# Kernel tuning notes

Hardware: AMD Instinct MI355X
Metric: run time of the kernel (lower is better)

## Reference

```python
import jax, jax.numpy as jnp
import numpy as np

# ---- structural constants (mirror e3nn SO3.tensor_productRs bookkeeping) ----
MUL = 2                      # multiplicity of every irrep in Rs_in / Rs_out
LS = [0, 1, 2]               # irrep orders present in Rs_in and Rs_out
L_MAX = 2                    # spherical-harmonics cutoff -> Y_dim = 9
N_BASIS, HIDDEN = 64, 64     # radial model sizes
R_MAX, GAMMA = 3.5, 4.0      # gaussian radial basis params


def _filter_paths():
    """One entry (l_filter) per (mul_out, mul_in, l_in, l_out, l_f) path."""
    paths = []
    for l_in in LS:
        for l_out in LS:
            for lf in range(abs(l_in - l_out), min(l_in + l_out, L_MAX) + 1):
                paths.extend([lf] * (MUL * MUL))  # mul_in * mul_out copies
    return paths  # len == n_path == 60


def _build_mix_matrices():
    """rf_mix[K, n_path]: broadcast each radial path weight over its 2l+1 components.
    ylm_mix[K, 9]: select Y_{l,m} for each filter component. Both 0/1, block sparse."""
    paths = _filter_paths()
    n_path = len(paths)
    K = sum(2 * l + 1 for l in paths)          # 204
    y_off = {0: 0, 1: 1, 2: 4}                 # offset of l-block inside Y (dim 9)
    rf = np.zeros((K, n_path), dtype=np.float32)
    ylm = np.zeros((K, 9), dtype=np.float32)
    k = 0
    for p, l in enumerate(paths):
        for m in range(2 * l + 1):
            rf[k, p] = 1.0
            ylm[k, y_off[l] + m] = 1.0
            k += 1
    return rf, ylm, n_path, K


def _sh_l012(n):
    """Real spherical harmonics l=0..2 on unit vectors n[Z,3] -> Y[9, Z]."""
    x, y, z = n[:, 0], n[:, 1], n[:, 2]
    c0 = 0.28209479177387814   # 1/(2 sqrt(pi))
    c1 = 0.4886025119029199    # sqrt(3/(4 pi))
    c2a = 1.0925484305920792   # sqrt(15/(4 pi))
    c2b = 0.31539156525252005  # sqrt(5/(16 pi))
    c2c = 0.5462742152960396   # sqrt(15/(16 pi))
    one = jnp.ones_like(x)
    return jnp.stack([
        c0 * one,
        c1 * y, c1 * z, c1 * x,
        c2a * x * y, c2a * y * z, c2b * (3.0 * z * z - 1.0), c2a * x * z,
        c2c * (x * x - y * y),
    ], axis=0)


def setup_inputs() -> dict:
    key = jax.random.key(0)
    k_r, k_cg, k_w1, k_w2 = jax.random.split(key, 4)
    Z = 65536
    D = MUL * sum(2 * l + 1 for l in LS)       # 18 (dim_in == dim_out)
    rf_np, ylm_np, n_path, K = _build_mix_matrices()
    r = 2.0 * jax.random.normal(k_r, (Z, 3), dtype=jnp.float32)
    cg = jax.random.normal(k_cg, (K, D, D), dtype=jnp.float32) / np.sqrt(K)
    W1 = jax.random.normal(k_w1, (N_BASIS, HIDDEN), dtype=jnp.float32) / np.sqrt(N_BASIS)
    b1 = jnp.zeros((HIDDEN,), dtype=jnp.float32)
    W2 = jax.random.normal(k_w2, (HIDDEN, n_path), dtype=jnp.float32) / np.sqrt(HIDDEN)
    b2 = jnp.zeros((n_path,), dtype=jnp.float32)
    return {"r": r, "W1": W1, "b1": b1, "W2": W2, "b2": b2,
            "cg": cg, "rf_mix": jnp.asarray(rf_np), "ylm_mix": jnp.asarray(ylm_np)}


def reference(r, W1, b1, W2, b2, cg, rf_mix, ylm_mix):
    radii = jnp.linalg.norm(r, axis=1)                    # [Z]
    n = r / (radii[:, None] + 1e-12)                      # unit directions
    Y = _sh_l012(n)                                       # [9, Z]  (sh returns [m, ...])
    centers = jnp.linspace(0.0, R_MAX, N_BASIS, dtype=jnp.float32)
    B = jnp.exp(-GAMMA * (radii[:, None] - centers) ** 2) # gaussian radial basis [Z, 64]
    R = jax.nn.relu(B @ W1 + b1) @ W2 + b2                # RadialModel -> [Z, n_path]
    Rm = jnp.einsum('kp,zp->zk', rf_mix, R)               # 'ij,zj->zi'
    Ym = jnp.einsum('ky,yz->zk', ylm_mix, Y)              # 'ij,jz->zi'
    # 'kij,zk,zk->zij' : fuse the two per-point vectors, then one GEMM over k
    kernel = jnp.einsum('kij,zk->zij', cg, Rm * Ym)       # [Z, 18, 18]
    return kernel
```

## Files before the change

kernel.cpp:

```cpp
#include <hip/hip_runtime.h>

#define NPATH 60
#define KDIM  204
#define KPAD  224
#define NIJ   324
#define NTIL  21
#define HID   64

#define BHS   88
#define CLS   232

typedef short bf16x8 __attribute__((ext_vector_type(8)));
typedef float f32x4  __attribute__((ext_vector_type(4)));

__device__ __align__(16) unsigned short g_w1s[4096];
__device__ __align__(16) unsigned short g_w2s[4096];
__device__ __align__(16) unsigned short g_cgs[75264];
__device__ unsigned int  g_pyk[112];

__device__ inline unsigned short f2bf(float f) {
    unsigned int u = __builtin_bit_cast(unsigned int, f);
    u += 0x7fffu + ((u >> 16) & 1u);
    return (unsigned short)(u >> 16);
}
__device__ inline float bf2f(unsigned short h) {
    unsigned int u = ((unsigned int)h) << 16;
    return __builtin_bit_cast(float, u);
}

__global__ void prep_kernel(const float* __restrict__ W1, const float* __restrict__ W2,
                            const float* __restrict__ cg, const float* __restrict__ rf,
                            const float* __restrict__ ylm)
{
    int idx = blockIdx.x * 256 + threadIdx.x;
    if (idx < 4096) {
        int e = idx & 7, ln = (idx >> 3) & 63, nt = (idx >> 9) & 3, kc = idx >> 11;
        int k = kc * 32 + (ln >> 4) * 8 + e;
        int n = nt * 16 + (ln & 15);
        g_w1s[idx] = f2bf(W1[k * HID + n]);
    } else if (idx < 8192) {
        int j = idx - 4096;
        int e = j & 7, ln = (j >> 3) & 63, nt = (j >> 9) & 3, kc = j >> 11;
        int k = kc * 32 + (ln >> 4) * 8 + e;
        int n = nt * 16 + (ln & 15);
        g_w2s[j] = f2bf(n < NPATH ? W2[k * NPATH + n] : 0.0f);
    } else if (idx < 8192 + 75264) {
        int j = idx - 8192;
        int e = j & 7, ln = (j >> 3) & 63;
        int nt = (j >> 9) % NTIL;
        int kc = j / (512 * NTIL);
        int k = kc * 32 + (ln >> 4) * 8 + e;
        int n = nt * 16 + (ln & 15);
        g_cgs[j] = f2bf((k < KDIM && n < NIJ) ? cg[k * NIJ + n] : 0.0f);
    } else if (idx < 8192 + 75264 + 112) {
        int j = idx - (8192 + 75264);
        int k0 = 2 * j, k1 = 2 * j + 1;
        unsigned p0 = 0, y0 = 0, p1 = 0, y1 = 0;
        if (k0 < KDIM) {
            for (int q = 0; q < NPATH; q++) if (rf[k0 * NPATH + q] != 0.0f) p0 = q;
            for (int q = 0; q < 9; q++)     if (ylm[k0 * 9 + q]   != 0.0f) y0 = q;
            for (int q = 0; q < NPATH; q++) if (rf[k1 * NPATH + q] != 0.0f) p1 = q;
            for (int q = 0; q < 9; q++)     if (ylm[k1 * 9 + q]   != 0.0f) y1 = q;
        }
        g_pyk[j] = p0 | (y0 << 8) | (p1 << 16) | (y1 << 24);
    }
}

union SmemU {
    struct {
        unsigned short Blds[64][BHS];
        unsigned short Hlds[64][BHS];
    } p1;
    unsigned short Clds[64][CLS];
};

__global__ __launch_bounds__(256) void fused_kernel(
    const float* __restrict__ r, const float* __restrict__ b1,
    const float* __restrict__ b2, float* __restrict__ out)
{
    __shared__ SmemU sm;
    __shared__ unsigned short Rl[64][61];
    __shared__ float Yl[64][9];
    __shared__ unsigned int pyL[112];

    const int tid  = threadIdx.x;
    const int wv   = tid >> 6;
    const int lane = tid & 63;
    const int quad = lane >> 4;
    const int l16  = lane & 15;
    const int z0   = blockIdx.x * 64;

    if (tid < 112) pyL[tid] = g_pyk[tid];
    if (tid < 64) {
        int z = z0 + tid;
        float x = r[z * 3 + 0], y = r[z * 3 + 1], zc = r[z * 3 + 2];
        float rad = sqrtf(x * x + y * y + zc * zc);
        float inv = 1.0f / (rad + 1e-12f);
        float nx = x * inv, ny = y * inv, nz = zc * inv;
        const float c0 = 0.28209479177387814f, c1 = 0.4886025119029199f;
        const float c2a = 1.0925484305920792f, c2b = 0.31539156525252005f, c2c = 0.5462742152960396f;
        Yl[tid][0] = c0;
        Yl[tid][1] = c1 * ny;
        Yl[tid][2] = c1 * nz;
        Yl[tid][3] = c1 * nx;
        Yl[tid][4] = c2a * nx * ny;
        Yl[tid][5] = c2a * ny * nz;
        Yl[tid][6] = c2b * (3.0f * nz * nz - 1.0f);
        Yl[tid][7] = c2a * nx * nz;
        Yl[tid][8] = c2c * (nx * nx - ny * ny);
    }
    {
        int zz = tid >> 2, grp = tid & 3;
        int z = z0 + zz;
        float x = r[z * 3 + 0], y = r[z * 3 + 1], zc = r[z * 3 + 2];
        float rad = sqrtf(x * x + y * y + zc * zc);
        const float step = 3.5f / 63.0f;
        const float NL2E = -5.770780163555852f;
        unsigned int* dst = (unsigned int*)&sm.p1.Blds[zz][grp * 16];
        #pragma unroll
        for (int ii = 0; ii < 8; ii++) {
            int i0 = grp * 16 + ii * 2;
            float d0 = rad - (float)i0 * step;
            float d1 = rad - (float)(i0 + 1) * step;
            unsigned int u0 = f2bf(__builtin_amdgcn_exp2f(d0 * d0 * NL2E));
            unsigned int u1 = f2bf(__builtin_amdgcn_exp2f(d1 * d1 * NL2E));
            dst[ii] = u0 | (u1 << 16);
        }
    }
    __syncthreads();

    {
        bf16x8 a0 = *(const bf16x8*)&sm.p1.Blds[wv * 16 + l16][0 + quad * 8];
        bf16x8 a1 = *(const bf16x8*)&sm.p1.Blds[wv * 16 + l16][32 + quad * 8];
        #pragma unroll
        for (int nt = 0; nt < 4; nt++) {
            bf16x8 bb0 = *(const bf16x8*)&g_w1s[((0 * 4 + nt) * 64 + lane) * 8];
            bf16x8 bb1 = *(const bf16x8*)&g_w1s[((1 * 4 + nt) * 64 + lane) * 8];
            f32x4 acc = {0.f, 0.f, 0.f, 0.f};
            acc = __builtin_amdgcn_mfma_f32_16x16x32_bf16(a0, bb0, acc, 0, 0, 0);
            acc = __builtin_amdgcn_mfma_f32_16x16x32_bf16(a1, bb1, acc, 0, 0, 0);
            int h = nt * 16 + l16;
            float bias = b1[h];
            #pragma unroll
            for (int rr = 0; rr < 4; rr++) {
                float v = acc[rr] + bias;
                v = v > 0.0f ? v : 0.0f;
                sm.p1.Hlds[wv * 16 + quad * 4 + rr][h] = f2bf(v);
            }
        }
    }
    __syncthreads();

    {
        bf16x8 a0 = *(const bf16x8*)&sm.p1.Hlds[wv * 16 + l16][0 + quad * 8];
        bf16x8 a1 = *(const bf16x8*)&sm.p1.Hlds[wv * 16 + l16][32 + quad * 8];
        #pragma unroll
        for (int nt = 0; nt < 4; nt++) {
            bf16x8 bb0 = *(const bf16x8*)&g_w2s[((0 * 4 + nt) * 64 + lane) * 8];
            bf16x8 bb1 = *(const bf16x8*)&g_w2s[((1 * 4 + nt) * 64 + lane) * 8];
            f32x4 acc = {0.f, 0.f, 0.f, 0.f};
            acc = __builtin_amdgcn_mfma_f32_16x16x32_bf16(a0, bb0, acc, 0, 0, 0);
            acc = __builtin_amdgcn_mfma_f32_16x16x32_bf16(a1, bb1, acc, 0, 0, 0);
            int p = nt * 16 + l16;
            if (p < NPATH) {
                float bias = b2[p];
                #pragma unroll
                for (int rr = 0; rr < 4; rr++)
                    Rl[wv * 16 + quad * 4 + rr][p] = f2bf(acc[rr] + bias);
            }
        }
    }
    __syncthreads();

    {
        const int j0 = wv * 28;
        char* rowp = (char*)&sm.Clds[lane][0];
        const unsigned key = ((lane >> 3) & 3) << 4;
        #pragma unroll
        for (int jj = 0; jj < 28; ++jj) {
            int j = j0 + jj;
            int k = 2 * j;
            unsigned u = 0;
            if (k < KDIM) {
                unsigned py = pyL[j];
                float cA = bf2f(Rl[lane][py & 255])         * Yl[lane][(py >> 8) & 255];
                float cB = bf2f(Rl[lane][(py >> 16) & 255]) * Yl[lane][(py >> 24)];
                u = (unsigned int)f2bf(cA) | ((unsigned int)f2bf(cB) << 16);
            }
            *(unsigned int*)(rowp + (((unsigned)(2 * k)) ^ key)) = u;
        }
    }
    __syncthreads();

    const int ntb = wv * 5 + (wv > 0 ? 1 : 0);
    const int cnt = (wv == 0) ? 6 : 5;

    #pragma unroll
    for (int half = 0; half < 2; half++) {
        f32x4 acc[3][4];
        #pragma unroll
        for (int ii = 0; ii < 3; ii++)
            #pragma unroll
            for (int zt = 0; zt < 4; zt++)
                acc[ii][zt] = (f32x4){0.f, 0.f, 0.f, 0.f};

        #pragma unroll
        for (int kc = 0; kc < 7; kc++) {
            bf16x8 az[4];
            #pragma unroll
            for (int zt = 0; zt < 4; zt++) {
                int z = zt * 16 + l16;
                unsigned boff = ((unsigned)(kc * 64 + quad * 16)) ^ (((unsigned)((z >> 3) & 3)) << 4);
                az[zt] = *(const bf16x8*)((const char*)&sm.Clds[z][0] + boff);
            }
            bf16x8 bg[3];
            #pragma unroll
            for (int ii = 0; ii < 3; ii++) {
                int nt = ntb + half * 3 + ii; if (nt > NTIL - 1) nt = NTIL - 1;
                bg[ii] = *(const bf16x8*)&g_cgs[((kc * NTIL + nt) * 64 + lane) * 8];
            }
            #pragma unroll
            for (int ii = 0; ii < 3; ii++) {
                if (half * 3 + ii < cnt) {
                    #pragma unroll
                    for (int zt = 0; zt < 4; zt++)
                        acc[ii][zt] = __builtin_amdgcn_mfma_f32_16x16x32_bf16(az[zt], bg[ii], acc[ii][zt], 0, 0, 0);
                }
            }
        }

        #pragma unroll
        for (int ii = 0; ii < 3; ii++) {
            if (half * 3 + ii < cnt) {
                int col = (ntb + half * 3 + ii) * 16 + l16;
                if (col < NIJ) {
                    #pragma unroll
                    for (int zt = 0; zt < 4; zt++) {
                        #pragma unroll
                        for (int rr = 0; rr < 4; rr++)
                            out[(z0 + zt * 16 + quad * 4 + rr) * NIJ + col] = acc[ii][zt][rr];
                    }
                }
            }
        }
    }
}

extern "C" void kernel_launch(void* const* d_in, const int* in_sizes, int n_in,
                              void* d_out, int out_size, void* d_ws, size_t ws_size,
                              hipStream_t stream) {
    const float* r   = (const float*)d_in[0];
    const float* W1  = (const float*)d_in[1];
    const float* b1  = (const float*)d_in[2];
    const float* W2  = (const float*)d_in[3];
    const float* b2  = (const float*)d_in[4];
    const float* cg  = (const float*)d_in[5];
    const float* rf  = (const float*)d_in[6];
    const float* ylm = (const float*)d_in[7];
    float* out = (float*)d_out;

    const int Z = in_sizes[0] / 3;

    prep_kernel<<<327, 256, 0, stream>>>(W1, W2, cg, rf, ylm);
    fused_kernel<<<Z / 64, 256, 0, stream>>>(r, b1, b2, out);
}
```

Measured before the change: 139.4 us.

## Make radial MLP stages wave-private to drop block barriers

Each wave now owns 16 points and keeps its own hidden, radial and spherical-harmonic scratch in a per-wave shared-memory slot. The gaussian basis is computed straight into MFMA operand registers, so its LDS round trip goes away. Three block-wide __syncthreads are replaced by s_waitcnt plus sched_barrier inside the wave, leaving one block barrier before the CG GEMM, which reads the C tiles of all four waves. Each lane now loads r and computes the radius itself, and the C-tile swizzle changes to a per-wave 224-wide layout, which could add LDS bank conflicts.

```diff
diff --git a/kernel.cpp b/kernel.cpp
--- a/kernel.cpp
+++ b/kernel.cpp
@@ -2,13 +2,9 @@
 
 #define NPATH 60
 #define KDIM  204
-#define KPAD  224
 #define NIJ   324
 #define NTIL  21
 #define HID   64
-
-#define BHS   88
-#define CLS   232
 
 typedef short bf16x8 __attribute__((ext_vector_type(8)));
 typedef float f32x4  __attribute__((ext_vector_type(4)));
@@ -66,22 +62,21 @@
     }
 }
 
-union SmemU {
-    struct {
-        unsigned short Blds[64][BHS];
-        unsigned short Hlds[64][BHS];
-    } p1;
-    unsigned short Clds[64][CLS];
+struct __align__(16) WaveMem {
+    union {
+        unsigned short Hw[16][88];
+        unsigned short Cw[16][224];
+    } u;
+    unsigned short Rw[16][61];
+    float          Yw[16][9];
 };
 
 __global__ __launch_bounds__(256) void fused_kernel(
     const float* __restrict__ r, const float* __restrict__ b1,
     const float* __restrict__ b2, float* __restrict__ out)
 {
-    __shared__ SmemU sm;
-    __shared__ unsigned short Rl[64][61];
-    __shared__ float Yl[64][9];
-    __shared__ unsigned int pyL[112];
+    __shared__ WaveMem wm[4];
+    __shared__ unsigned int pyw[112];
 
     const int tid  = threadIdx.x;
     const int wv   = tid >> 6;
@@ -90,110 +85,112 @@
     const int l16  = lane & 15;
     const int z0   = blockIdx.x * 64;
 
-    if (tid < 112) pyL[tid] = g_pyk[tid];
-    if (tid < 64) {
-        int z = z0 + tid;
-        float x = r[z * 3 + 0], y = r[z * 3 + 1], zc = r[z * 3 + 2];
-        float rad = sqrtf(x * x + y * y + zc * zc);
+    pyw[lane] = g_pyk[lane];
+    if (lane < 48) pyw[64 + lane] = g_pyk[64 + lane];
+
+    const int zloc = wv * 16 + l16;
+    const int zg   = z0 + zloc;
+    float x = r[zg * 3 + 0], y = r[zg * 3 + 1], zc = r[zg * 3 + 2];
+    float rad = sqrtf(x * x + y * y + zc * zc);
+
+    if (quad == 0) {
         float inv = 1.0f / (rad + 1e-12f);
         float nx = x * inv, ny = y * inv, nz = zc * inv;
         const float c0 = 0.28209479177387814f, c1 = 0.4886025119029199f;
         const float c2a = 1.0925484305920792f, c2b = 0.31539156525252005f, c2c = 0.5462742152960396f;
-        Yl[tid][0] = c0;
-        Yl[tid][1] = c1 * ny;
-        Yl[tid][2] = c1 * nz;
-        Yl[tid][3] = c1 * nx;
-        Yl[tid][4] = c2a * nx * ny;
-        Yl[tid][5] = c2a * ny * nz;
-        Yl[tid][6] = c2b * (3.0f * nz * nz - 1.0f);
-        Yl[tid][7] = c2a * nx * nz;
-        Yl[tid][8] = c2c * (nx * nx - ny * ny);
-    }
+        wm[wv].Yw[l16][0] = c0;
+        wm[wv].Yw[l16][1] = c1 * ny;
+        wm[wv].Yw[l16][2] = c1 * nz;
+        wm[wv].Yw[l16][3] = c1 * nx;
+        wm[wv].Yw[l16][4] = c2a * nx * ny;
+        wm[wv].Yw[l16][5] = c2a * ny * nz;
+        wm[wv].Yw[l16][6] = c2b * (3.0f * nz * nz - 1.0f);
+        wm[wv].Yw[l16][7] = c2a * nx * nz;
+        wm[wv].Yw[l16][8] = c2c * (nx * nx - ny * ny);
+    }
+
+    union { bf16x8 v; unsigned int d[4]; } A0, A1;
     {
-        int zz = tid >> 2, grp = tid & 3;
-        int z = z0 + zz;
-        float x = r[z * 3 + 0], y = r[z * 3 + 1], zc = r[z * 3 + 2];
-        float rad = sqrtf(x * x + y * y + zc * zc);
         const float step = 3.5f / 63.0f;
         const float NL2E = -5.770780163555852f;
-        unsigned int* dst = (unsigned int*)&sm.p1.Blds[zz][grp * 16];
-        #pragma unroll
-        for (int ii = 0; ii < 8; ii++) {
-            int i0 = grp * 16 + ii * 2;
+        #pragma unroll
+        for (int ii = 0; ii < 4; ii++) {
+            int i0 = quad * 8 + 2 * ii;
             float d0 = rad - (float)i0 * step;
             float d1 = rad - (float)(i0 + 1) * step;
-            unsigned int u0 = f2bf(__builtin_amdgcn_exp2f(d0 * d0 * NL2E));
-            unsigned int u1 = f2bf(__builtin_amdgcn_exp2f(d1 * d1 * NL2E));
-            dst[ii] = u0 | (u1 << 16);
-        }
-    }
-    __syncthreads();
+            A0.d[ii] = (unsigned)f2bf(__builtin_amdgcn_exp2f(d0 * d0 * NL2E))
+                     | ((unsigned)f2bf(__builtin_amdgcn_exp2f(d1 * d1 * NL2E)) << 16);
+            int i2 = 32 + i0;
+            float e0 = rad - (float)i2 * step;
+            float e1 = rad - (float)(i2 + 1) * step;
+            A1.d[ii] = (unsigned)f2bf(__builtin_amdgcn_exp2f(e0 * e0 * NL2E))
+                     | ((unsigned)f2bf(__builtin_amdgcn_exp2f(e1 * e1 * NL2E)) << 16);
+        }
+    }
+
+    #pragma unroll
+    for (int nt = 0; nt < 4; nt++) {
+        bf16x8 bb0 = *(const bf16x8*)&g_w1s[((0 * 4 + nt) * 64 + lane) * 8];
+        bf16x8 bb1 = *(const bf16x8*)&g_w1s[((1 * 4 + nt) * 64 + lane) * 8];
+        f32x4 acc = {0.f, 0.f, 0.f, 0.f};
+        acc = __builtin_amdgcn_mfma_f32_16x16x32_bf16(A0.v, bb0, acc, 0, 0, 0);
+        acc = __builtin_amdgcn_mfma_f32_16x16x32_bf16(A1.v, bb1, acc, 0, 0, 0);
+        int h = nt * 16 + l16;
+        float bias = b1[h];
+        #pragma unroll
+        for (int rr = 0; rr < 4; rr++) {
+            float v = acc[rr] + bias;
+            v = v > 0.0f ? v : 0.0f;
+            wm[wv].u.Hw[quad * 4 + rr][h] = f2bf(v);
+        }
+    }
+    asm volatile("s_waitcnt lgkmcnt(0)" ::: "memory");
+    __builtin_amdgcn_sched_barrier(0);
 
     {
-        bf16x8 a0 = *(const bf16x8*)&sm.p1.Blds[wv * 16 + l16][0 + quad * 8];
-        bf16x8 a1 = *(const bf16x8*)&sm.p1.Blds[wv * 16 + l16][32 + quad * 8];
-        #pragma unroll
-        for (int nt = 0; nt < 4; nt++) {
-            bf16x8 bb0 = *(const bf16x8*)&g_w1s[((0 * 4 + nt) * 64 + lane) * 8];
-            bf16x8 bb1 = *(const bf16x8*)&g_w1s[((1 * 4 + nt) * 64 + lane) * 8];
-            f32x4 acc = {0.f, 0.f, 0.f, 0.f};
-            acc = __builtin_amdgcn_mfma_f32_16x16x32_bf16(a0, bb0, acc, 0, 0, 0);
-            acc = __builtin_amdgcn_mfma_f32_16x16x32_bf16(a1, bb1, acc, 0, 0, 0);
-            int h = nt * 16 + l16;
-            float bias = b1[h];
-            #pragma unroll
-            for (int rr = 0; rr < 4; rr++) {
-                float v = acc[rr] + bias;
-                v = v > 0.0f ? v : 0.0f;
-                sm.p1.Hlds[wv * 16 + quad * 4 + rr][h] = f2bf(v);
-            }
-        }
-    }
-    __syncthreads();
-
-    {
-        bf16x8 a0 = *(const bf16x8*)&sm.p1.Hlds[wv * 16 + l16][0 + quad * 8];
-        bf16x8 a1 = *(const bf16x8*)&sm.p1.Hlds[wv * 16 + l16][32 + quad * 8];
+        bf16x8 h0 = *(const bf16x8*)&wm[wv].u.Hw[l16][0 + quad * 8];
+        bf16x8 h1 = *(const bf16x8*)&wm[wv].u.Hw[l16][32 + quad * 8];
         #pragma unroll
         for (int nt = 0; nt < 4; nt++) {
             bf16x8 bb0 = *(const bf16x8*)&g_w2s[((0 * 4 + nt) * 64 + lane) * 8];
             bf16x8 bb1 = *(const bf16x8*)&g_w2s[((1 * 4 + nt) * 64 + lane) * 8];
             f32x4 acc = {0.f, 0.f, 0.f, 0.f};
-            acc = __builtin_amdgcn_mfma_f32_16x16x32_bf16(a0, bb0, acc, 0, 0, 0);
-            acc = __builtin_amdgcn_mfma_f32_16x16x32_bf16(a1, bb1, acc, 0, 0, 0);
+            acc = __builtin_amdgcn_mfma_f32_16x16x32_bf16(h0, bb0, acc, 0, 0, 0);
+            acc = __builtin_amdgcn_mfma_f32_16x16x32_bf16(h1, bb1, acc, 0, 0, 0);
             int p = nt * 16 + l16;
             if (p < NPATH) {
                 float bias = b2[p];
                 #pragma unroll
                 for (int rr = 0; rr < 4; rr++)
-                    Rl[wv * 16 + quad * 4 + rr][p] = f2bf(acc[rr] + bias);
-            }
-        }
-    }
-    __syncthreads();
+                    wm[wv].Rw[quad * 4 + rr][p] = f2bf(acc[rr] + bias);
+            }
+        }
+    }
+    asm volatile("s_waitcnt lgkmcnt(0)" ::: "memory");
+    __builtin_amdgcn_sched_barrier(0);
 
     {
-        const int j0 = wv * 28;
-        char* rowp = (char*)&sm.Clds[lane][0];
-        const unsigned key = ((lane >> 3) & 3) << 4;
-        #pragma unroll
-        for (int jj = 0; jj < 28; ++jj) {
-            int j = j0 + jj;
-            int k = 2 * j;
+        const unsigned gkey = ((unsigned)((l16 >> 2) & 3)) << 2;
+        unsigned int* crow = (unsigned int*)&wm[wv].u.Cw[l16][0];
+        #pragma unroll
+        for (int jj = 0; jj < 28; jj++) {
+            int j = quad * 28 + jj;
             unsigned u = 0;
-            if (k < KDIM) {
-                unsigned py = pyL[j];
-                float cA = bf2f(Rl[lane][py & 255])         * Yl[lane][(py >> 8) & 255];
-                float cB = bf2f(Rl[lane][(py >> 16) & 255]) * Yl[lane][(py >> 24)];
-                u = (unsigned int)f2bf(cA) | ((unsigned int)f2bf(cB) << 16);
-            }
-            *(unsigned int*)(rowp + (((unsigned)(2 * k)) ^ key)) = u;
-        }
-    }
+            if (2 * j < KDIM) {
+                unsigned py = pyw[j];
+                float cA = bf2f(wm[wv].Rw[l16][py & 255])          * wm[wv].Yw[l16][(py >> 8) & 255];
+                float cB = bf2f(wm[wv].Rw[l16][(py >> 16) & 255])  * wm[wv].Yw[l16][py >> 24];
+                u = (unsigned)f2bf(cA) | ((unsigned)f2bf(cB) << 16);
+            }
+            crow[j ^ gkey] = u;
+        }
+    }
+
     __syncthreads();
 
     const int ntb = wv * 5 + (wv > 0 ? 1 : 0);
     const int cnt = (wv == 0) ? 6 : 5;
+    const unsigned bkey = ((unsigned)((l16 >> 2) & 3)) << 4;
 
     #pragma unroll
     for (int half = 0; half < 2; half++) {
@@ -209,9 +206,8 @@
             bf16x8 az[4];
             #pragma unroll
             for (int zt = 0; zt < 4; zt++) {
-                int z = zt * 16 + l16;
-                unsigned boff = ((unsigned)(kc * 64 + quad * 16)) ^ (((unsigned)((z >> 3) & 3)) << 4);
-                az[zt] = *(const bf16x8*)((const char*)&sm.Clds[z][0] + boff);
+                unsigned boff = ((unsigned)(kc * 64 + quad * 16)) ^ bkey;
+                az[zt] = *(const bf16x8*)((const char*)&wm[zt].u.Cw[l16][0] + boff);
             }
             bf16x8 bg[3];
             #pragma unroll
```

New measurement: 138.2 us. About the same (-0.9%).
